# Performance work log

Measured on AMD Instinct MI355X. Metric: run time of the kernel, lower is better.

Reference implementation:

```python
import jax, jax.numpy as jnp
import numpy as np

B, T, J, D = 2048, 120, 24, 6
E = J * D            # embed_dim = 144
L = 4                # n_layer
NH = 8               # n_head
HD = E // NH         # head_dim = 18
H = 144              # d_model = gru hidden (must equal E, see forward concat)
FF = 4 * E           # transformer dim_feedforward
GIN = E + H          # gru input size


def _layernorm(x, w, b):
    m = x.mean(-1, keepdims=True)
    v = ((x - m) ** 2).mean(-1, keepdims=True)
    return (x - m) / jnp.sqrt(v + 1e-5) * w + b


def setup_inputs() -> dict:
    key = jax.random.key(0)
    ks = jax.random.split(key, 32)
    s = 0.02
    n = lambda k, sh: jax.random.normal(k, sh, jnp.float32) * s
    return {
        "seed": jax.random.normal(ks[0], (B, T, J, D), jnp.float32),
        "qkv_w": n(ks[1], (L, 3 * E, E)), "qkv_b": jnp.zeros((L, 3 * E), jnp.float32),
        "out_w": n(ks[2], (L, E, E)), "out_b": jnp.zeros((L, E), jnp.float32),
        "ln1_w": jnp.ones((L, E), jnp.float32), "ln1_b": jnp.zeros((L, E), jnp.float32),
        "ffn1_w": n(ks[3], (L, FF, E)), "ffn1_b": jnp.zeros((L, FF), jnp.float32),
        "ffn2_w": n(ks[4], (L, E, FF)), "ffn2_b": jnp.zeros((L, E), jnp.float32),
        "ln2_w": jnp.ones((L, E), jnp.float32), "ln2_b": jnp.zeros((L, E), jnp.float32),
        "proj_w": n(ks[5], (E, E)), "proj_b": jnp.zeros((E,), jnp.float32),
        "w_ih": n(ks[6], (3 * H, GIN)), "w_hh": n(ks[7], (3 * H, H)),
        "b_ih": jnp.zeros((3 * H,), jnp.float32), "b_hh": jnp.zeros((3 * H,), jnp.float32),
        "spl_w": n(ks[8], (E, H)), "spl_b": jnp.zeros((E,), jnp.float32),
        "future": 24,
    }


def reference(seed, qkv_w, qkv_b, out_w, out_b, ln1_w, ln1_b, ffn1_w, ffn1_b,
              ffn2_w, ffn2_b, ln2_w, ln2_b, proj_w, proj_b,
              w_ih, w_hh, b_ih, b_hh, spl_w, spl_b, future):
    Bv, Tv, Jv, Dv = seed.shape
    x = seed.reshape(Bv, Tv, Jv * Dv)  # [B, T, E]

    # --- TransformerEncoder (post-norm, relu, dropout=eval-mode identity) ---
    def layer_step(x, p):
        (qw, qb, ow, ob, l1w, l1b, f1w, f1b, f2w, f2b, l2w, l2b) = p
        qkv = jnp.einsum('bse,fe->bsf', x, qw) + qb          # [B,S,3E]
        q, k, v = jnp.split(qkv, 3, axis=-1)
        q = q.reshape(Bv, Tv, NH, HD)
        k = k.reshape(Bv, Tv, NH, HD)
        v = v.reshape(Bv, Tv, NH, HD)
        scores = jnp.einsum('bqhd,bkhd->bhqk', q, k) / jnp.sqrt(jnp.float32(HD))
        attn = jax.nn.softmax(scores, axis=-1)
        o = jnp.einsum('bhqk,bkhd->bqhd', attn, v).reshape(Bv, Tv, E)
        o = jnp.einsum('bse,fe->bsf', o, ow) + ob
        x = _layernorm(x + o, l1w, l1b)
        ff = jax.nn.relu(jnp.einsum('bse,fe->bsf', x, f1w) + f1b)
        ff = jnp.einsum('bsf,ef->bse', ff, f2w) + f2b
        x = _layernorm(x + ff, l2w, l2b)
        return x, None

    x, _ = jax.lax.scan(layer_step, x,
                        (qkv_w, qkv_b, out_w, out_b, ln1_w, ln1_b,
                         ffn1_w, ffn1_b, ffn2_w, ffn2_b, ln2_w, ln2_b))
    ctx = x.mean(axis=1) @ proj_w.T + proj_b               # [B, E]

    h0 = jnp.zeros((Bv, H), seed.dtype)
    inp0 = seed[:, -1].reshape(Bv, Jv * Dv)

    def step(carry, _):
        h, inp = carry
        xc = jnp.concatenate([inp, ctx], axis=-1)          # [B, E+H]
        gi = xc @ w_ih.T + b_ih                            # [B, 3H]
        gh = h @ w_hh.T + b_hh
        ir, iz, in_ = jnp.split(gi, 3, axis=-1)
        hr, hz, hn = jnp.split(gh, 3, axis=-1)
        r = jax.nn.sigmoid(ir + hr)
        z = jax.nn.sigmoid(iz + hz)
        n = jnp.tanh(in_ + r * hn)
        h_new = (1.0 - z) * n + z * h
        rot6d = h_new @ spl_w.T + spl_b                    # [B, E]
        return (h_new, rot6d), rot6d

    _, ys = jax.lax.scan(step, (h0, inp0), None, length=future)  # [future,B,E]
    return ys.transpose(1, 0, 2).reshape(Bv, future, Jv, Dv)
```

## Files before the change

### kernel.cpp

```cpp
#include <hip/hip_runtime.h>

#define B_   2048
#define T_   120
#define E_   144
#define L_   4
#define NH_  8
#define HD_  18
#define FF_  576
#define H_   144
#define GIN_ 288
#define TH_  432
#define FUT_ 24
#define BT_  (B_*T_)

typedef unsigned short u16;
typedef unsigned int   u32;

typedef __attribute__((ext_vector_type(8))) short short8v;
typedef __attribute__((ext_vector_type(4))) float f32x4;

__device__ __forceinline__ float bf2f(u16 u) {
    u32 x = ((u32)u) << 16;
    return __uint_as_float(x);
}
__device__ __forceinline__ u16 f2bf(float f) {
    u32 x = __float_as_uint(f);
    u32 r = (x + 0x7fffu + ((x >> 16) & 1u)) >> 16;
    return (u16)r;
}

struct F4 { float x, y, z, w; };

__device__ __forceinline__ F4 load4(const float* p) {
    float4 v = *(const float4*)p;
    return {v.x, v.y, v.z, v.w};
}
__device__ __forceinline__ void store1(float* p, float v) { *p = v; }
__device__ __forceinline__ void store1(u16* p, float v)   { *p = f2bf(v); }

__device__ __forceinline__ short8v wfrag(const u16* Wp, int tile, int NS, int s, int l) {
    return *(const short8v*)(Wp + (((size_t)tile * NS + s) * 64 + l) * 8);
}

__device__ __forceinline__ void gll16(const void* g, void* l) {
    __builtin_amdgcn_global_load_lds(
        (const __attribute__((address_space(1))) u32*)g,
        (__attribute__((address_space(3))) u32*)l, 16, 0, 0);
}

__device__ __forceinline__ void stage64(const u16* src, u32* lds, int tid) {
    const char* base = (const char*)src;
    char* lbase = (char*)lds;
    const int w = tid >> 6, l = tid & 63;
#pragma unroll
    for (int i = 0; i < 7; ++i) {
        int inst  = w * 7 + i;
        int chunk = inst * 64 + l;
        int row = chunk / 21;
        int col = chunk - row * 21;
        if (col > 17) col = 17;
        gll16(base + row * 288 + col * 16, lbase + inst * 1024);
    }
}

__global__ void wpack_kernel(const float* __restrict__ src, u16* __restrict__ dst,
                             int ntiles, int NS, int K, int sstr)
{
    int i = blockIdx.x * 256 + threadIdx.x;
    if (i >= ntiles * NS * 512) return;
    int e  = i & 7;
    int l  = (i >> 3) & 63;
    int c  = i >> 9;
    int s  = c % NS;
    int tile = c / NS;
    int li = l & 15, lg = l >> 4;
    int row = tile * 16 + li;
    int k   = s * 32 + lg * 8 + e;
    dst[i] = (k < K) ? f2bf(src[(size_t)row * sstr + k]) : (u16)0;
}

__global__ void cast_bf_kernel(const float* __restrict__ src, u16* __restrict__ dst,
                               int n2)
{
    int i = blockIdx.x * 256 + threadIdx.x;
    if (i >= n2) return;
    float2 t = ((const float2*)src)[i];
    ((u32*)dst)[i] = ((u32)f2bf(t.y) << 16) | (u32)f2bf(t.x);
}

template<typename OT>
__global__ __launch_bounds__(192) void gemm_mfma(
    const u16* __restrict__ A, const u16* __restrict__ Wb,
    const float* __restrict__ bias, OT* __restrict__ C, int M, int N)
{
    __shared__ u32 lds[64 * 84];

    const int tid = threadIdx.x;
    const int w   = tid >> 6;
    const int l   = tid & 63;
    const int lg  = l >> 4;
    const int li  = l & 15;
    const int bm  = blockIdx.y * 64;
    const int n0w = blockIdx.x * 144 + w * 48;
    const int t0  = blockIdx.x * 9 + w * 3;

    f32x4 acc[4][3];
#pragma unroll
    for (int rt = 0; rt < 4; rt++)
#pragma unroll
        for (int ct = 0; ct < 3; ct++) acc[rt][ct] = {0.f, 0.f, 0.f, 0.f};

    stage64(A + (size_t)bm * 144, lds, tid);
    __syncthreads();

    const u16* lds16 = (const u16*)lds;
#pragma unroll
    for (int s = 0; s < 5; ++s) {
        short8v bf[3];
#pragma unroll
        for (int ct = 0; ct < 3; ++ct)
            bf[ct] = wfrag(Wb, t0 + ct, 5, s, l);
        short8v af[4];
#pragma unroll
        for (int rt = 0; rt < 4; ++rt)
            af[rt] = *(const short8v*)(lds16 + (rt * 16 + li) * 168 + s * 32 + lg * 8);
#pragma unroll
        for (int rt = 0; rt < 4; ++rt)
#pragma unroll
            for (int ct = 0; ct < 3; ++ct)
                acc[rt][ct] = __builtin_amdgcn_mfma_f32_16x16x32_bf16(
                    af[rt], bf[ct], acc[rt][ct], 0, 0, 0);
    }

#pragma unroll
    for (int ct = 0; ct < 3; ++ct) {
        int col = n0w + ct * 16 + li;
        float bv = bias[col];
#pragma unroll
        for (int rt = 0; rt < 4; ++rt) {
#pragma unroll
            for (int j = 0; j < 4; ++j) {
                int row = bm + rt * 16 + lg * 4 + j;
                store1(&C[(size_t)row * N + col], acc[rt][ct][j] + bv);
            }
        }
    }
}

template<bool RESBF, bool WF32>
__global__ __launch_bounds__(192) void olnffn_kernel(
    const u16* __restrict__ ob, const u16* __restrict__ Wo,
    const float* __restrict__ ob_b,
    const float* __restrict__ resf, const u16* __restrict__ resb,
    const float* __restrict__ ln1w, const float* __restrict__ ln1b,
    const u16* __restrict__ W1, const float* __restrict__ b1,
    const u16* __restrict__ W2, const float* __restrict__ b2,
    const float* __restrict__ ln2w, const float* __restrict__ ln2b,
    u16* __restrict__ obf, float* __restrict__ of)
{
    __shared__ __align__(16) u16 Als[64 * 168];
    __shared__ u32 Fls[64 * 52];
    __shared__ float lnS[3][64], lnQ[3][64];

    const int tid = threadIdx.x;
    const int w   = tid >> 6;
    const int l   = tid & 63;
    const int lg  = l >> 4;
    const int li  = l & 15;
    const int bm  = blockIdx.x * 64;

    stage64(ob + (size_t)bm * 144, (u32*)Als, tid);

    float rr[4][3][4];
#pragma unroll
    for (int ct = 0; ct < 3; ++ct) {
        int col = w * 48 + ct * 16 + li;
#pragma unroll
        for (int rt = 0; rt < 4; ++rt)
#pragma unroll
            for (int j = 0; j < 4; ++j) {
                int row = bm + rt * 16 + lg * 4 + j;
                rr[rt][ct][j] = RESBF ? bf2f(resb[(size_t)row * E_ + col])
                                      : resf[(size_t)row * E_ + col];
            }
    }
    __syncthreads();

    const u16* als = Als;
    u16* alsw = Als;
    u16* fls16 = (u16*)Fls;

    f32x4 acc[4][3];
#pragma unroll
    for (int rt = 0; rt < 4; rt++)
#pragma unroll
        for (int ct = 0; ct < 3; ct++) acc[rt][ct] = {0.f, 0.f, 0.f, 0.f};
#pragma unroll
    for (int s = 0; s < 5; ++s) {
        short8v bf[3];
#pragma unroll
        for (int ct = 0; ct < 3; ++ct)
            bf[ct] = wfrag(Wo, w * 3 + ct, 5, s, l);
        short8v af[4];
#pragma unroll
        for (int rt = 0; rt < 4; ++rt)
            af[rt] = *(const short8v*)(als + (rt * 16 + li) * 168 + s * 32 + lg * 8);
#pragma unroll
        for (int rt = 0; rt < 4; ++rt)
#pragma unroll
            for (int ct = 0; ct < 3; ++ct)
                acc[rt][ct] = __builtin_amdgcn_mfma_f32_16x16x32_bf16(
                    af[rt], bf[ct], acc[rt][ct], 0, 0, 0);
    }

    float vv[4][3][4];
#pragma unroll
    for (int ct = 0; ct < 3; ++ct) {
        int col = w * 48 + ct * 16 + li;
        float bv = ob_b[col];
#pragma unroll
        for (int rt = 0; rt < 4; ++rt)
#pragma unroll
            for (int j = 0; j < 4; ++j)
                vv[rt][ct][j] = acc[rt][ct][j] + bv + rr[rt][ct][j];
    }
#pragma unroll
    for (int rt = 0; rt < 4; ++rt)
#pragma unroll
        for (int j = 0; j < 4; ++j) {
            float s = vv[rt][0][j] + vv[rt][1][j] + vv[rt][2][j];
            float q = vv[rt][0][j] * vv[rt][0][j] + vv[rt][1][j] * vv[rt][1][j]
                    + vv[rt][2][j] * vv[rt][2][j];
#pragma unroll
            for (int off = 1; off < 16; off <<= 1) {
                s += __shfl_xor(s, off);
                q += __shfl_xor(q, off);
            }
            if (li == 0) {
                lnS[w][rt * 16 + lg * 4 + j] = s;
                lnQ[w][rt * 16 + lg * 4 + j] = q;
            }
        }
    __syncthreads();
#pragma unroll
    for (int rt = 0; rt < 4; ++rt)
#pragma unroll
        for (int j = 0; j < 4; ++j) {
            int r = rt * 16 + lg * 4 + j;
            float mean = (lnS[0][r] + lnS[1][r] + lnS[2][r]) * (1.f / 144.f);
            float var  = (lnQ[0][r] + lnQ[1][r] + lnQ[2][r]) * (1.f / 144.f) - mean * mean;
            float rstd = rsqrtf(var + 1e-5f);
#pragma unroll
            for (int ct = 0; ct < 3; ++ct) {
                int col = w * 48 + ct * 16 + li;
                float o = (vv[rt][ct][j] - mean) * rstd * ln1w[col] + ln1b[col];
                vv[rt][ct][j] = o;
                alsw[r * 168 + col] = f2bf(o);
            }
        }
    __syncthreads();

    f32x4 acc2[4][3];
#pragma unroll
    for (int rt = 0; rt < 4; rt++)
#pragma unroll
        for (int ct = 0; ct < 3; ct++) acc2[rt][ct] = {0.f, 0.f, 0.f, 0.f};

    for (int c = 0; c < 6; ++c) {
        f32x4 acc1[4][2];
#pragma unroll
        for (int rt = 0; rt < 4; rt++)
#pragma unroll
            for (int ct = 0; ct < 2; ct++) acc1[rt][ct] = {0.f, 0.f, 0.f, 0.f};
#pragma unroll
        for (int s = 0; s < 5; ++s) {
            short8v bf[2];
#pragma unroll
            for (int ct = 0; ct < 2; ++ct)
                bf[ct] = wfrag(W1, c * 6 + w * 2 + ct, 5, s, l);
            short8v af[4];
#pragma unroll
            for (int rt = 0; rt < 4; ++rt)
                af[rt] = *(const short8v*)(als + (rt * 16 + li) * 168 + s * 32 + lg * 8);
#pragma unroll
            for (int rt = 0; rt < 4; ++rt)
#pragma unroll
                for (int ct = 0; ct < 2; ++ct)
                    acc1[rt][ct] = __builtin_amdgcn_mfma_f32_16x16x32_bf16(
                        af[rt], bf[ct], acc1[rt][ct], 0, 0, 0);
        }
        __syncthreads();
#pragma unroll
        for (int ct = 0; ct < 2; ++ct) {
            int colc = w * 32 + ct * 16 + li;
            float bv = b1[c * 96 + colc];
#pragma unroll
            for (int rt = 0; rt < 4; ++rt)
#pragma unroll
                for (int j = 0; j < 4; ++j) {
                    int row = rt * 16 + lg * 4 + j;
                    float v = fmaxf(acc1[rt][ct][j] + bv, 0.f);
                    fls16[row * 104 + colc] = f2bf(v);
                }
        }
        __syncthreads();
#pragma unroll
        for (int s2 = 0; s2 < 3; ++s2) {
            short8v wf[3];
#pragma unroll
            for (int ct = 0; ct < 3; ++ct)
                wf[ct] = wfrag(W2, w * 3 + ct, 18, c * 3 + s2, l);
            short8v pf[4];
#pragma unroll
            for (int rt = 0; rt < 4; ++rt)
                pf[rt] = *(const short8v*)(fls16 + (rt * 16 + li) * 104 + s2 * 32 + lg * 8);
#pragma unroll
            for (int rt = 0; rt < 4; ++rt)
#pragma unroll
                for (int ct = 0; ct < 3; ++ct)
                    acc2[rt][ct] = __builtin_amdgcn_mfma_f32_16x16x32_bf16(
                        pf[rt], wf[ct], acc2[rt][ct], 0, 0, 0);
        }
    }

    float v2[4][3][4];
#pragma unroll
    for (int ct = 0; ct < 3; ++ct) {
        int col = w * 48 + ct * 16 + li;
        float bv = b2[col];
#pragma unroll
        for (int rt = 0; rt < 4; ++rt)
#pragma unroll
            for (int j = 0; j < 4; ++j)
                v2[rt][ct][j] = acc2[rt][ct][j] + bv + vv[rt][ct][j];
    }
#pragma unroll
    for (int rt = 0; rt < 4; ++rt)
#pragma unroll
        for (int j = 0; j < 4; ++j) {
            float s = v2[rt][0][j] + v2[rt][1][j] + v2[rt][2][j];
            float q = v2[rt][0][j] * v2[rt][0][j] + v2[rt][1][j] * v2[rt][1][j]
                    + v2[rt][2][j] * v2[rt][2][j];
#pragma unroll
            for (int off = 1; off < 16; off <<= 1) {
                s += __shfl_xor(s, off);
                q += __shfl_xor(q, off);
            }
            if (li == 0) {
                lnS[w][rt * 16 + lg * 4 + j] = s;
                lnQ[w][rt * 16 + lg * 4 + j] = q;
            }
        }
    __syncthreads();
#pragma unroll
    for (int rt = 0; rt < 4; ++rt)
#pragma unroll
        for (int j = 0; j < 4; ++j) {
            int r = rt * 16 + lg * 4 + j;
            float mean = (lnS[0][r] + lnS[1][r] + lnS[2][r]) * (1.f / 144.f);
            float var  = (lnQ[0][r] + lnQ[1][r] + lnQ[2][r]) * (1.f / 144.f) - mean * mean;
            float rstd = rsqrtf(var + 1e-5f);
            int row = bm + r;
#pragma unroll
            for (int ct = 0; ct < 3; ++ct) {
                int col = w * 48 + ct * 16 + li;
                float o = (v2[rt][ct][j] - mean) * rstd * ln2w[col] + ln2b[col];
                obf[(size_t)row * E_ + col] = f2bf(o);
                if (WF32) of[(size_t)row * E_ + col] = o;
            }
        }
}

template<typename AT, typename OT, bool BIAS, bool RELU, bool RES>
__global__ __launch_bounds__(256) void gemm_kernel(
    const AT* __restrict__ A, const float* __restrict__ W, int ldw,
    const float* __restrict__ bias, const float* __restrict__ res,
    OT* __restrict__ C, int M, int N, int K)
{
    constexpr int BM = 64, BN = 64, BK = 16;
    __shared__ float As[BK][BM + 4];
    __shared__ float Ws[BK][BN + 4];
    const int tid = threadIdx.x;
    const int bm = blockIdx.y * BM;
    const int bn = blockIdx.x * BN;
    const int tx = tid & 15, ty = tid >> 4;
    const int lr = tid >> 2;
    const int lc = (tid & 3) << 2;

    float acc[4][4];
#pragma unroll
    for (int i = 0; i < 4; i++)
#pragma unroll
        for (int j = 0; j < 4; j++) acc[i][j] = 0.f;

    for (int k0 = 0; k0 < K; k0 += BK) {
        F4 av = load4(A + (size_t)(bm + lr) * K + k0 + lc);
        As[lc + 0][lr] = av.x; As[lc + 1][lr] = av.y;
        As[lc + 2][lr] = av.z; As[lc + 3][lr] = av.w;
        int n = bn + lr;
        F4 wv = {0.f, 0.f, 0.f, 0.f};
        if (n < N) {
            float4 t = *(const float4*)(W + (size_t)n * ldw + k0 + lc);
            wv = {t.x, t.y, t.z, t.w};
        }
        Ws[lc + 0][lr] = wv.x; Ws[lc + 1][lr] = wv.y;
        Ws[lc + 2][lr] = wv.z; Ws[lc + 3][lr] = wv.w;
        __syncthreads();
#pragma unroll
        for (int kk = 0; kk < BK; ++kk) {
            float a[4], wr[4];
#pragma unroll
            for (int i = 0; i < 4; i++) a[i] = As[kk][ty * 4 + i];
#pragma unroll
            for (int j = 0; j < 4; j++) wr[j] = Ws[kk][tx * 4 + j];
#pragma unroll
            for (int i = 0; i < 4; i++)
#pragma unroll
                for (int j = 0; j < 4; j++) acc[i][j] += a[i] * wr[j];
        }
        __syncthreads();
    }
#pragma unroll
    for (int i = 0; i < 4; i++) {
        int m = bm + ty * 4 + i;
#pragma unroll
        for (int j = 0; j < 4; j++) {
            int n = bn + tx * 4 + j;
            if (n < N) {
                float v = acc[i][j];
                if (BIAS) v += bias[n];
                if (RES)  v += res[(size_t)m * N + n];
                if (RELU) v = fmaxf(v, 0.f);
                store1(&C[(size_t)m * N + n], v);
            }
        }
    }
}

__global__ __launch_bounds__(256) void attn_kernel(const u16* __restrict__ qkv,
                                                   u16* __restrict__ o)
{
    constexpr int QS = 40;
    constexpr int VS = 136;
    __shared__ __align__(16) u16 Qs[128 * QS];
    __shared__ __align__(16) u16 Ks[128 * QS];
    __shared__ __align__(16) u16 Vt[32 * VS];
    __shared__ __align__(16) u16 Ps[4][16 * VS];

    const int bh = blockIdx.x;
    const int b = bh >> 3, h = bh & 7;
    const int tid = threadIdx.x;
    const int w = tid >> 6, l = tid & 63;
    const int lg = l >> 4, li = l & 15;

    {
        u32* z1 = (u32*)Qs;
        for (int i = tid; i < 128 * QS / 2; i += 256) z1[i] = 0;
        u32* z2 = (u32*)Ks;
        for (int i = tid; i < 128 * QS / 2; i += 256) z2[i] = 0;
        u32* z3 = (u32*)Vt;
        for (int i = tid; i < 32 * VS / 2; i += 256) z3[i] = 0;
    }
    __syncthreads();

    const u32* q32 = (const u32*)(qkv + (size_t)b * T_ * TH_);
    for (int idx = tid; idx < 120 * 9; idx += 256) {
        int t = idx / 9, dp = idx - t * 9;
        u32 qv = q32[t * 216 + 9 * h + dp];
        u32 kv = q32[t * 216 + 72 + 9 * h + dp];
        u32 vv = q32[t * 216 + 144 + 9 * h + dp];
        ((u32*)(Qs + t * QS))[dp] = qv;
        ((u32*)(Ks + t * QS))[dp] = kv;
        Vt[(2 * dp) * VS + t]     = (u16)(vv & 0xffffu);
        Vt[(2 * dp + 1) * VS + t] = (u16)(vv >> 16);
    }
    __syncthreads();

    const float scale = 0.23570226039551584f;
    u16* pw = &Ps[w][0];

    for (int mt = w * 2; mt < w * 2 + 2; ++mt) {
        short8v qf = *(const short8v*)(Qs + (mt * 16 + li) * QS + lg * 8);
        f32x4 sacc[8];
#pragma unroll
        for (int nt = 0; nt < 8; ++nt) sacc[nt] = {0.f, 0.f, 0.f, 0.f};
#pragma unroll
        for (int nt = 0; nt < 8; ++nt) {
            short8v kf = *(const short8v*)(Ks + (nt * 16 + li) * QS + lg * 8);
            sacc[nt] = __builtin_amdgcn_mfma_f32_16x16x32_bf16(qf, kf, sacc[nt], 0, 0, 0);
        }

        float invl[4];
#pragma unroll
        for (int j = 0; j < 4; ++j) {
            float v[8];
            float m = -1e30f;
#pragma unroll
            for (int nt = 0; nt < 8; ++nt) {
                float s = sacc[nt][j] * scale;
                if (nt == 7 && li >= 8) s = -1e30f;
                v[nt] = s;
                m = fmaxf(m, s);
            }
#pragma unroll
            for (int off = 1; off < 16; off <<= 1)
                m = fmaxf(m, __shfl_xor(m, off));
            float sum = 0.f;
#pragma unroll
            for (int nt = 0; nt < 8; ++nt) {
                float p = __expf(v[nt] - m);
                sum += p;
                pw[(lg * 4 + j) * VS + nt * 16 + li] = f2bf(p);
            }
#pragma unroll
            for (int off = 1; off < 16; off <<= 1)
                sum += __shfl_xor(sum, off);
            invl[j] = 1.f / sum;
        }

        f32x4 oacc[2] = {{0.f,0.f,0.f,0.f},{0.f,0.f,0.f,0.f}};
#pragma unroll
        for (int s = 0; s < 4; ++s) {
            short8v pf = *(const short8v*)(pw + li * VS + s * 32 + lg * 8);
#pragma unroll
            for (int dt = 0; dt < 2; ++dt) {
                short8v vf = *(const short8v*)(Vt + (dt * 16 + li) * VS + s * 32 + lg * 8);
                oacc[dt] = __builtin_amdgcn_mfma_f32_16x16x32_bf16(pf, vf, oacc[dt], 0, 0, 0);
            }
        }

        const int q0 = mt * 16 + lg * 4;
#pragma unroll
        for (int dt = 0; dt < 2; ++dt) {
            int d = dt * 16 + li;
            if (d < HD_) {
#pragma unroll
                for (int j = 0; j < 4; ++j) {
                    int q = q0 + j;
                    if (q < T_)
                        o[((size_t)b * T_ + q) * E_ + h * HD_ + d] =
                            f2bf(oacc[dt][j] * invl[j]);
                }
            }
        }
    }
}

__global__ void mean_kernel(const float* __restrict__ x, float* __restrict__ out,
                            int nb)
{
    int idx = blockIdx.x * blockDim.x + threadIdx.x;
    if (idx >= nb * E_) return;
    int b = idx / E_, e = idx % E_;
    const float* p = x + (size_t)b * T_ * E_ + e;
    float s = 0.f;
    for (int t = 0; t < T_; t++) s += p[(size_t)t * E_];
    out[idx] = s * (1.f / 120.f);
}

__device__ __forceinline__ float sigmoidf_(float x) {
    return 1.f / (1.f + __expf(-x));
}

#define GRU_M 16
__global__ __launch_bounds__(192) void gru_all_kernel(
    const float* __restrict__ seed,
    const float* __restrict__ gctx,
    const u16* __restrict__ WxB,
    const u16* __restrict__ WhB,
    const u16* __restrict__ SpB,
    const float* __restrict__ b_hh,
    const float* __restrict__ spl_b,
    float* __restrict__ out)
{
    __shared__ __align__(16) u16 xls[GRU_M * 168];
    __shared__ __align__(16) u16 hls[GRU_M * 168];

    const int tid = threadIdx.x;
    const int w = tid >> 6, l = tid & 63;
    const int lg = l >> 4, li = l & 15;
    const int b0 = blockIdx.x * GRU_M;
    const int fr = w * 48 + li;

    for (int i = tid; i < GRU_M * 84; i += 192) {
        ((u32*)xls)[i] = 0; ((u32*)hls)[i] = 0;
    }
    __syncthreads();
    for (int i = tid; i < GRU_M * 72; i += 192) {
        int r = i / 72, e2 = i - r * 72;
        float2 t = *(const float2*)(seed + (size_t)(b0 + r) * T_ * E_
                                    + (size_t)(T_ - 1) * E_ + 2 * e2);
        ((u32*)(xls + r * 168))[e2] = ((u32)f2bf(t.y) << 16) | (u32)f2bf(t.x);
    }

    float gctxv[3][3][4];
    float bhh[3][3];
    float splb[3];
#pragma unroll
    for (int g = 0; g < 3; ++g)
#pragma unroll
        for (int ct = 0; ct < 3; ++ct) {
            int f = g * 144 + fr + ct * 16;
            bhh[g][ct] = b_hh[f];
#pragma unroll
            for (int j = 0; j < 4; ++j)
                gctxv[g][ct][j] = gctx[(size_t)(b0 + lg * 4 + j) * TH_ + f];
        }
#pragma unroll
    for (int ct = 0; ct < 3; ++ct) splb[ct] = spl_b[fr + ct * 16];

    float hold[3][4];
#pragma unroll
    for (int ct = 0; ct < 3; ++ct)
#pragma unroll
        for (int j = 0; j < 4; ++j) hold[ct][j] = 0.f;

    __syncthreads();

    for (int st = 0; st < FUT_; ++st) {
        f32x4 aRZ[2][3], aNi[3], aNh[3];
#pragma unroll
        for (int g = 0; g < 2; ++g)
#pragma unroll
            for (int ct = 0; ct < 3; ++ct) aRZ[g][ct] = {0.f, 0.f, 0.f, 0.f};
#pragma unroll
        for (int ct = 0; ct < 3; ++ct) {
            aNi[ct] = {0.f, 0.f, 0.f, 0.f};
            aNh[ct] = {0.f, 0.f, 0.f, 0.f};
        }
#pragma unroll
        for (int s = 0; s < 5; ++s) {
            short8v ax = *(const short8v*)(xls + li * 168 + s * 32 + lg * 8);
            short8v ah = *(const short8v*)(hls + li * 168 + s * 32 + lg * 8);
#pragma unroll
            for (int ct = 0; ct < 3; ++ct) {
#pragma unroll
                for (int g = 0; g < 2; ++g) {
                    int tile = g * 9 + w * 3 + ct;
                    short8v bx = wfrag(WxB, tile, 5, s, l);
                    aRZ[g][ct] = __builtin_amdgcn_mfma_f32_16x16x32_bf16(ax, bx, aRZ[g][ct], 0, 0, 0);
                    short8v bh = wfrag(WhB, tile, 5, s, l);
                    aRZ[g][ct] = __builtin_amdgcn_mfma_f32_16x16x32_bf16(ah, bh, aRZ[g][ct], 0, 0, 0);
                }
                int tile2 = 18 + w * 3 + ct;
                short8v bx2 = wfrag(WxB, tile2, 5, s, l);
                aNi[ct] = __builtin_amdgcn_mfma_f32_16x16x32_bf16(ax, bx2, aNi[ct], 0, 0, 0);
                short8v bh2 = wfrag(WhB, tile2, 5, s, l);
                aNh[ct] = __builtin_amdgcn_mfma_f32_16x16x32_bf16(ah, bh2, aNh[ct], 0, 0, 0);
            }
        }
        __syncthreads();
#pragma unroll
        for (int ct = 0; ct < 3; ++ct)
#pragma unroll
            for (int j = 0; j < 4; ++j) {
                float r = sigmoidf_(aRZ[0][ct][j] + gctxv[0][ct][j] + bhh[0][ct]);
                float z = sigmoidf_(aRZ[1][ct][j] + gctxv[1][ct][j] + bhh[1][ct]);
                float n = tanhf(aNi[ct][j] + gctxv[2][ct][j]
                                + r * (aNh[ct][j] + bhh[2][ct]));
                float hv = (1.f - z) * n + z * hold[ct][j];
                hold[ct][j] = hv;
                hls[(lg * 4 + j) * 168 + fr + ct * 16] = f2bf(hv);
            }
        __syncthreads();
        f32x4 aS[3];
#pragma unroll
        for (int ct = 0; ct < 3; ++ct) aS[ct] = {0.f, 0.f, 0.f, 0.f};
#pragma unroll
        for (int s = 0; s < 5; ++s) {
            short8v ah = *(const short8v*)(hls + li * 168 + s * 32 + lg * 8);
#pragma unroll
            for (int ct = 0; ct < 3; ++ct) {
                short8v bs = wfrag(SpB, w * 3 + ct, 5, s, l);
                aS[ct] = __builtin_amdgcn_mfma_f32_16x16x32_bf16(ah, bs, aS[ct], 0, 0, 0);
            }
        }
#pragma unroll
        for (int ct = 0; ct < 3; ++ct) {
            int col = fr + ct * 16;
#pragma unroll
            for (int j = 0; j < 4; ++j) {
                float rv = aS[ct][j] + splb[ct];
                out[(size_t)(b0 + lg * 4 + j) * (FUT_ * E_) + (size_t)st * E_ + col] = rv;
                xls[(lg * 4 + j) * 168 + col] = f2bf(rv);
            }
        }
        __syncthreads();
    }
}

extern "C" void kernel_launch(void* const* d_in, const int* in_sizes, int n_in,
                              void* d_out, int out_size, void* d_ws, size_t ws_size,
                              hipStream_t stream)
{
    const float* seed   = (const float*)d_in[0];
    const float* qkv_w  = (const float*)d_in[1];
    const float* qkv_b  = (const float*)d_in[2];
    const float* out_w  = (const float*)d_in[3];
    const float* out_b  = (const float*)d_in[4];
    const float* ln1_w  = (const float*)d_in[5];
    const float* ln1_b  = (const float*)d_in[6];
    const float* ffn1_w = (const float*)d_in[7];
    const float* ffn1_b = (const float*)d_in[8];
    const float* ffn2_w = (const float*)d_in[9];
    const float* ffn2_b = (const float*)d_in[10];
    const float* ln2_w  = (const float*)d_in[11];
    const float* ln2_b  = (const float*)d_in[12];
    const float* proj_w = (const float*)d_in[13];
    const float* proj_b = (const float*)d_in[14];
    const float* w_ih   = (const float*)d_in[15];
    const float* w_hh   = (const float*)d_in[16];
    const float* b_ih   = (const float*)d_in[17];
    const float* b_hh   = (const float*)d_in[18];
    const float* spl_w  = (const float*)d_in[19];
    const float* spl_b  = (const float*)d_in[20];

    const size_t qkvW_n  = (size_t)L_ * TH_ * 160;
    const size_t outW_n  = (size_t)L_ * E_ * 160;
    const size_t ffn1W_n = (size_t)L_ * FF_ * 160;
    const size_t ffn2W_n = (size_t)L_ * E_ * 576;
    const size_t wxW_n   = (size_t)TH_ * 160;
    const size_t whW_n   = (size_t)TH_ * 160;
    const size_t spW_n   = (size_t)E_ * 160;
    const size_t wbytes  = (qkvW_n + outW_n + ffn1W_n + ffn2W_n
                            + wxW_n + whW_n + spW_n) * 2;

    const size_t persist = (size_t)B_ * 4 * (E_ + E_ + TH_) + wbytes;

    int nc = 16;
    for (int c = 1; c <= 16; c <<= 1) {
        size_t rows = (size_t)(B_ / c) * T_;
        size_t need = persist + rows * 2016;
        if (need <= ws_size) { nc = c; break; }
    }
    const int BC = B_ / nc;
    const int CR = BC * T_;

    char* wsp = (char*)d_ws;
    u16*   xbf   = (u16*)wsp;   wsp += (size_t)CR * E_ * 2;
    float* xres  = (float*)wsp; wsp += (size_t)CR * E_ * 4;
    u16*   qf    = (u16*)wsp;   wsp += (size_t)CR * TH_ * 2;
    u16*   ob    = (u16*)wsp;   wsp += (size_t)CR * E_ * 2;
    float* ctxm  = (float*)wsp; wsp += (size_t)B_ * E_ * 4;
    float* ctx   = (float*)wsp; wsp += (size_t)B_ * E_ * 4;
    float* gctx  = (float*)wsp; wsp += (size_t)B_ * TH_ * 4;
    u16* qkvWb   = (u16*)wsp;   wsp += qkvW_n * 2;
    u16* outWb   = (u16*)wsp;   wsp += outW_n * 2;
    u16* ffn1Wb  = (u16*)wsp;   wsp += ffn1W_n * 2;
    u16* ffn2Wb  = (u16*)wsp;   wsp += ffn2W_n * 2;
    u16* wxB     = (u16*)wsp;   wsp += wxW_n * 2;
    u16* whB     = (u16*)wsp;   wsp += whW_n * 2;
    u16* splWb   = (u16*)wsp;   wsp += spW_n * 2;

    wpack_kernel<<<(int)((qkvW_n + 255) / 256), 256, 0, stream>>>(qkv_w, qkvWb, L_ * 27, 5, 144, 144);
    wpack_kernel<<<(int)((outW_n + 255) / 256), 256, 0, stream>>>(out_w, outWb, L_ * 9, 5, 144, 144);
    wpack_kernel<<<(int)((ffn1W_n + 255) / 256), 256, 0, stream>>>(ffn1_w, ffn1Wb, L_ * 36, 5, 144, 144);
    wpack_kernel<<<(int)((ffn2W_n + 255) / 256), 256, 0, stream>>>(ffn2_w, ffn2Wb, L_ * 9, 18, 576, 576);
    wpack_kernel<<<(int)((wxW_n + 255) / 256), 256, 0, stream>>>(w_ih, wxB, 27, 5, 144, GIN_);
    wpack_kernel<<<(int)((whW_n + 255) / 256), 256, 0, stream>>>(w_hh, whB, 27, 5, 144, 144);
    wpack_kernel<<<(int)((spW_n + 255) / 256), 256, 0, stream>>>(spl_w, splWb, 9, 5, 144, 144);

    auto grid = [](int M, int N) { return dim3((N + 63) / 64, M / 64); };

    for (int c = 0; c < nc; c++) {
        const int b0 = c * BC;
        cast_bf_kernel<<<(CR * 72 + 255) / 256, 256, 0, stream>>>(
            seed + (size_t)b0 * T_ * E_, xbf, CR * 72);
        for (int l = 0; l < L_; l++) {
            gemm_mfma<u16><<<dim3(3, CR / 64), 192, 0, stream>>>(
                xbf, qkvWb + (size_t)l * TH_ * 160, qkv_b + (size_t)l * TH_,
                qf, CR, TH_);
            attn_kernel<<<BC * NH_, 256, 0, stream>>>(qf, ob);
            if (l == 0) {
                olnffn_kernel<false, false><<<CR / 64, 192, 0, stream>>>(
                    ob, outWb + (size_t)l * E_ * 160, out_b + (size_t)l * E_,
                    seed + (size_t)b0 * T_ * E_, nullptr,
                    ln1_w + (size_t)l * E_, ln1_b + (size_t)l * E_,
                    ffn1Wb + (size_t)l * FF_ * 160, ffn1_b + (size_t)l * FF_,
                    ffn2Wb + (size_t)l * E_ * 576, ffn2_b + (size_t)l * E_,
                    ln2_w + (size_t)l * E_, ln2_b + (size_t)l * E_, xbf, nullptr);
            } else if (l < 3) {
                olnffn_kernel<true, false><<<CR / 64, 192, 0, stream>>>(
                    ob, outWb + (size_t)l * E_ * 160, out_b + (size_t)l * E_,
                    nullptr, xbf,
                    ln1_w + (size_t)l * E_, ln1_b + (size_t)l * E_,
                    ffn1Wb + (size_t)l * FF_ * 160, ffn1_b + (size_t)l * FF_,
                    ffn2Wb + (size_t)l * E_ * 576, ffn2_b + (size_t)l * E_,
                    ln2_w + (size_t)l * E_, ln2_b + (size_t)l * E_, xbf, nullptr);
            } else {
                olnffn_kernel<true, true><<<CR / 64, 192, 0, stream>>>(
                    ob, outWb + (size_t)l * E_ * 160, out_b + (size_t)l * E_,
                    nullptr, xbf,
                    ln1_w + (size_t)l * E_, ln1_b + (size_t)l * E_,
                    ffn1Wb + (size_t)l * FF_ * 160, ffn1_b + (size_t)l * FF_,
                    ffn2Wb + (size_t)l * E_ * 576, ffn2_b + (size_t)l * E_,
                    ln2_w + (size_t)l * E_, ln2_b + (size_t)l * E_, xbf, xres);
            }
        }
        mean_kernel<<<(BC * E_ + 255) / 256, 256, 0, stream>>>(xres, ctxm + (size_t)b0 * E_, BC);
    }

    gemm_kernel<float, float, true, false, false><<<grid(B_, E_), 256, 0, stream>>>(
        ctxm, proj_w, E_, proj_b, nullptr, ctx, B_, E_, E_);
    gemm_kernel<float, float, true, false, false><<<grid(B_, TH_), 256, 0, stream>>>(
        ctx, w_ih + E_, GIN_, b_ih, nullptr, gctx, B_, TH_, E_);

    gru_all_kernel<<<B_ / GRU_M, 192, 0, stream>>>(
        seed, gctx, wxB, whB, splWb, b_hh, spl_b, (float*)d_out);
}
```

Measured before the change: 2.855 ms.

## Compute full QKV row tile per block and halve GRU batch per block

The QKV GEMM now uses one 256-thread block per 64-row tile covering all 432 output columns, instead of three 192-thread blocks that each restaged the same A tile. Each of the 4 waves handles interleaved column tiles, which removes redundant A loads and LDS staging at the cost of more accumulators per thread. Separately, the GRU decode kernel processes 8 batch rows per block instead of 16, doubling the number of blocks for more parallelism in the serial decode. The MFMA still computes 16 rows, so half of that work is masked out and wasted.

```diff
diff --git a/kernel.cpp b/kernel.cpp
--- a/kernel.cpp
+++ b/kernel.cpp
@@ -30,7 +30,6 @@
 }
 
 struct F4 { float x, y, z, w; };
-
 __device__ __forceinline__ F4 load4(const float* p) {
     float4 v = *(const float4*)p;
     return {v.x, v.y, v.z, v.w};
@@ -60,6 +59,23 @@
         int col = chunk - row * 21;
         if (col > 17) col = 17;
         gll16(base + row * 288 + col * 16, lbase + inst * 1024);
+    }
+}
+
+__device__ __forceinline__ void stage64_w4(const u16* src, u32* lds, int tid) {
+    const char* base = (const char*)src;
+    char* lbase = (char*)lds;
+    const int w = tid >> 6, l = tid & 63;
+#pragma unroll
+    for (int i = 0; i < 6; ++i) {
+        int inst = w * 6 + i;
+        if (inst < 21) {
+            int chunk = inst * 64 + l;
+            int row = chunk / 21;
+            int col = chunk - row * 21;
+            if (col > 17) col = 17;
+            gll16(base + row * 288 + col * 16, lbase + inst * 1024);
+        }
     }
 }
 
@@ -88,10 +104,9 @@
     ((u32*)dst)[i] = ((u32)f2bf(t.y) << 16) | (u32)f2bf(t.x);
 }
 
-template<typename OT>
-__global__ __launch_bounds__(192) void gemm_mfma(
+__global__ __launch_bounds__(256) void gemm_qkv(
     const u16* __restrict__ A, const u16* __restrict__ Wb,
-    const float* __restrict__ bias, OT* __restrict__ C, int M, int N)
+    const float* __restrict__ bias, u16* __restrict__ C, int M)
 {
     __shared__ u32 lds[64 * 84];
 
@@ -100,49 +115,50 @@
     const int l   = tid & 63;
     const int lg  = l >> 4;
     const int li  = l & 15;
-    const int bm  = blockIdx.y * 64;
-    const int n0w = blockIdx.x * 144 + w * 48;
-    const int t0  = blockIdx.x * 9 + w * 3;
-
-    f32x4 acc[4][3];
-#pragma unroll
-    for (int rt = 0; rt < 4; rt++)
-#pragma unroll
-        for (int ct = 0; ct < 3; ct++) acc[rt][ct] = {0.f, 0.f, 0.f, 0.f};
-
-    stage64(A + (size_t)bm * 144, lds, tid);
+    const int bm  = blockIdx.x * 64;
+
+    f32x4 acc[7][4];
+#pragma unroll
+    for (int ci = 0; ci < 7; ++ci)
+#pragma unroll
+        for (int rt = 0; rt < 4; ++rt) acc[ci][rt] = {0.f, 0.f, 0.f, 0.f};
+
+    stage64_w4(A + (size_t)bm * 144, lds, tid);
     __syncthreads();
 
     const u16* lds16 = (const u16*)lds;
 #pragma unroll
     for (int s = 0; s < 5; ++s) {
-        short8v bf[3];
-#pragma unroll
-        for (int ct = 0; ct < 3; ++ct)
-            bf[ct] = wfrag(Wb, t0 + ct, 5, s, l);
         short8v af[4];
 #pragma unroll
         for (int rt = 0; rt < 4; ++rt)
             af[rt] = *(const short8v*)(lds16 + (rt * 16 + li) * 168 + s * 32 + lg * 8);
 #pragma unroll
-        for (int rt = 0; rt < 4; ++rt)
-#pragma unroll
-            for (int ct = 0; ct < 3; ++ct)
-                acc[rt][ct] = __builtin_amdgcn_mfma_f32_16x16x32_bf16(
-                    af[rt], bf[ct], acc[rt][ct], 0, 0, 0);
-    }
-
-#pragma unroll
-    for (int ct = 0; ct < 3; ++ct) {
-        int col = n0w + ct * 16 + li;
-        float bv = bias[col];
-#pragma unroll
-        for (int rt = 0; rt < 4; ++rt) {
-#pragma unroll
-            for (int j = 0; j < 4; ++j) {
-                int row = bm + rt * 16 + lg * 4 + j;
-                store1(&C[(size_t)row * N + col], acc[rt][ct][j] + bv);
-            }
+        for (int ci = 0; ci < 7; ++ci) {
+            int ct = w + 4 * ci;
+            if (ct < 27) {
+                short8v bf = wfrag(Wb, ct, 5, s, l);
+#pragma unroll
+                for (int rt = 0; rt < 4; ++rt)
+                    acc[ci][rt] = __builtin_amdgcn_mfma_f32_16x16x32_bf16(
+                        af[rt], bf, acc[ci][rt], 0, 0, 0);
+            }
+        }
+    }
+
+#pragma unroll
+    for (int ci = 0; ci < 7; ++ci) {
+        int ct = w + 4 * ci;
+        if (ct < 27) {
+            int col = ct * 16 + li;
+            float bv = bias[col];
+#pragma unroll
+            for (int rt = 0; rt < 4; ++rt)
+#pragma unroll
+                for (int j = 0; j < 4; ++j) {
+                    int row = bm + rt * 16 + lg * 4 + j;
+                    C[(size_t)row * TH_ + col] = f2bf(acc[ci][rt][j] + bv);
+                }
         }
     }
 }
@@ -562,7 +578,7 @@
     return 1.f / (1.f + __expf(-x));
 }
 
-#define GRU_M 16
+#define GRU_M 8
 __global__ __launch_bounds__(192) void gru_all_kernel(
     const float* __restrict__ seed,
     const float* __restrict__ gctx,
@@ -573,16 +589,17 @@
     const float* __restrict__ spl_b,
     float* __restrict__ out)
 {
-    __shared__ __align__(16) u16 xls[GRU_M * 168];
-    __shared__ __align__(16) u16 hls[GRU_M * 168];
+    __shared__ __align__(16) u16 xls[16 * 168];
+    __shared__ __align__(16) u16 hls[16 * 168];
 
     const int tid = threadIdx.x;
     const int w = tid >> 6, l = tid & 63;
     const int lg = l >> 4, li = l & 15;
     const int b0 = blockIdx.x * GRU_M;
     const int fr = w * 48 + li;
-
-    for (int i = tid; i < GRU_M * 84; i += 192) {
+    const bool rowok = (lg < 2);
+
+    for (int i = tid; i < 16 * 84; i += 192) {
         ((u32*)xls)[i] = 0; ((u32*)hls)[i] = 0;
     }
     __syncthreads();
@@ -603,8 +620,11 @@
             int f = g * 144 + fr + ct * 16;
             bhh[g][ct] = b_hh[f];
 #pragma unroll
-            for (int j = 0; j < 4; ++j)
-                gctxv[g][ct][j] = gctx[(size_t)(b0 + lg * 4 + j) * TH_ + f];
+            for (int j = 0; j < 4; ++j) {
+                int rb = b0 + lg * 4 + j;
+                if (rb >= B_) rb = B_ - 1;
+                gctxv[g][ct][j] = gctx[(size_t)rb * TH_ + f];
+            }
         }
 #pragma unroll
     for (int ct = 0; ct < 3; ++ct) splb[ct] = spl_b[fr + ct * 16];
@@ -660,7 +680,8 @@
                                 + r * (aNh[ct][j] + bhh[2][ct]));
                 float hv = (1.f - z) * n + z * hold[ct][j];
                 hold[ct][j] = hv;
-                hls[(lg * 4 + j) * 168 + fr + ct * 16] = f2bf(hv);
+                if (rowok)
+                    hls[(lg * 4 + j) * 168 + fr + ct * 16] = f2bf(hv);
             }
         __syncthreads();
         f32x4 aS[3];
@@ -680,9 +701,11 @@
             int col = fr + ct * 16;
 #pragma unroll
             for (int j = 0; j < 4; ++j) {
-                float rv = aS[ct][j] + splb[ct];
-                out[(size_t)(b0 + lg * 4 + j) * (FUT_ * E_) + (size_t)st * E_ + col] = rv;
-                xls[(lg * 4 + j) * 168 + col] = f2bf(rv);
+                if (rowok) {
+                    float rv = aS[ct][j] + splb[ct];
+                    out[(size_t)(b0 + lg * 4 + j) * (FUT_ * E_) + (size_t)st * E_ + col] = rv;
+                    xls[(lg * 4 + j) * 168 + col] = f2bf(rv);
+                }
             }
         }
         __syncthreads();
@@ -767,9 +790,8 @@
         cast_bf_kernel<<<(CR * 72 + 255) / 256, 256, 0, stream>>>(
             seed + (size_t)b0 * T_ * E_, xbf, CR * 72);
         for (int l = 0; l < L_; l++) {
-            gemm_mfma<u16><<<dim3(3, CR / 64), 192, 0, stream>>>(
-                xbf, qkvWb + (size_t)l * TH_ * 160, qkv_b + (size_t)l * TH_,
-                qf, CR, TH_);
+            gemm_qkv<<<CR / 64, 256, 0, stream>>>(
+                xbf, qkvWb + (size_t)l * TH_ * 160, qkv_b + (size_t)l * TH_, qf, CR);
             attn_kernel<<<BC * NH_, 256, 0, stream>>>(qf, ob);
             if (l == 0) {
                 olnffn_kernel<false, false><<<CR / 64, 192, 0, stream>>>(
```

After: 2.927 ms. +2.5%, slower.
